# Kernel optimization log

Hardware: AMD Instinct MI355X
Metric: run time of the kernel (lower is better)

## Reference

```python
import jax, jax.numpy as jnp
import numpy as np

B, H, S, D = 8, 16, 1024, 64

def setup_inputs() -> dict:
    key = jax.random.key(0)
    k1, k2, k3, k4 = jax.random.split(key, 4)
    Q = jax.random.normal(k1, (B, H, S, D), dtype=jnp.float32)
    K = jax.random.normal(k2, (B, H, S, D), dtype=jnp.float32)
    V = jax.random.normal(k3, (B, H, S, D), dtype=jnp.float32)
    mask = jax.random.randint(k4, (B,), 0, 2).astype(jnp.bool_)
    return {"Q": Q, "K": K, "V": V, "mask": mask}

def reference(Q, K, V, mask):
    # scores: [B,H,S,S]
    scores = jnp.einsum('bhqd,bhkd->bhqk', Q, K)
    # per-batch-element mask broadcast over heads and both seq dims
    scores = jnp.where(mask[:, None, None, None], jnp.float32(-1e9), scores)
    # NOTE: original divides by sqrt(d) AFTER masking, so masked value is -1e9/sqrt(d)
    inv_sqrt_d = jnp.float32(1.0 / np.sqrt(Q.shape[-1]))
    attn = jax.nn.softmax(scores * inv_sqrt_d, axis=-1)
    return jnp.einsum('bhqk,bhkd->bhqd', attn, V)
```

## Files before the change

### kernel.cpp

```cpp
#include <hip/hip_runtime.h>
#include <hip/hip_bf16.h>

typedef __bf16 bf16;
typedef __bf16 bf16x4 __attribute__((ext_vector_type(4)));
typedef __bf16 bf16x8 __attribute__((ext_vector_type(8)));
typedef float  f32x16 __attribute__((ext_vector_type(16)));

#define S_  1024
#define D_  64
#define BQ  256
#define BK  64
#define KT  (S_/BK)
#define QT  (S_/BQ)
#define LD  72

#define ZERO16 {0.f,0.f,0.f,0.f,0.f,0.f,0.f,0.f,0.f,0.f,0.f,0.f,0.f,0.f,0.f,0.f}

__global__ __launch_bounds__(256, 2)
void fa_fwd(const float* __restrict__ Q, const float* __restrict__ K,
            const float* __restrict__ V, const int* __restrict__ mask,
            float* __restrict__ O)
{
    __shared__ bf16 ks[2][BK][LD];
    __shared__ bf16 vt[2][D_][LD];

    const int tid  = threadIdx.x;
    const int lane = tid & 63;
    const int w    = tid >> 6;
    const int l32  = lane & 31;
    const int hi   = lane >> 5;

    const int bid   = blockIdx.x;
    const int xcd   = bid & 7;
    const int rnd   = bid >> 3;
    const int qtile = rnd & 3;
    const int bh    = ((rnd >> 2) << 3) | xcd;
    const int b     = bh >> 4;
    const size_t base = (size_t)bh * (S_ * D_);
    const int qW = qtile * BQ + w * 64;

    const float qscale = (mask[b] != 0) ? 0.0f : 0.1803368801111204f;

    bf16x8 qf[2][4];
    #pragma unroll
    for (int nt = 0; nt < 2; ++nt) {
        const float* qp = Q + base + (size_t)(qW + nt * 32 + l32) * D_ + hi * 8;
        #pragma unroll
        for (int kc = 0; kc < 4; ++kc) {
            float4 a = *(const float4*)(qp + kc * 16);
            float4 c = *(const float4*)(qp + kc * 16 + 4);
            bf16x8 f;
            f[0] = (bf16)(a.x * qscale); f[1] = (bf16)(a.y * qscale);
            f[2] = (bf16)(a.z * qscale); f[3] = (bf16)(a.w * qscale);
            f[4] = (bf16)(c.x * qscale); f[5] = (bf16)(c.y * qscale);
            f[6] = (bf16)(c.z * qscale); f[7] = (bf16)(c.w * qscale);
            qf[nt][kc] = f;
        }
    }

    f32x16 o[2][2];
    #pragma unroll
    for (int dm = 0; dm < 2; ++dm)
        #pragma unroll
        for (int nt = 0; nt < 2; ++nt) o[dm][nt] = (f32x16)ZERO16;
    float lsum[2] = {0.f, 0.f};

    const int vkq = (tid >> 2) & 15;
    const int vkp = (vkq & 12) | ((vkq & 1) << 1) | ((vkq >> 1) & 1);
    const int vc4 = (tid & 3) + 4 * w;
    const float4* gk = (const float4*)(K + base);
    const float4* gv = (const float4*)(V + base);

    float4 kr[4], vr[4];
    #pragma unroll
    for (int it = 0; it < 4; ++it) kr[it] = gk[it * 256 + tid];
    #pragma unroll
    for (int r = 0; r < 4; ++r)    vr[r]  = gv[(vkq * 4 + r) * 16 + vc4];

    auto mkpf = [&](const f32x16& sv, bf16x8& fA, bf16x8& fB, float& ls) {
        bf16x8 a, c;
        #pragma unroll
        for (int i = 0; i < 8; ++i) {
            float e0 = __builtin_amdgcn_exp2f(sv[i]);
            float e1 = __builtin_amdgcn_exp2f(sv[8 + i]);
            ls += e0 + e1;
            a[i] = (bf16)e0;
            c[i] = (bf16)e1;
        }
        fA = a; fB = c;
    };

    for (int kt = 0; kt < KT; ++kt) {
        bf16 (*ksb)[LD] = ks[kt & 1];
        bf16 (*vtb)[LD] = vt[kt & 1];

        #pragma unroll
        for (int it = 0; it < 4; ++it) {
            int i = it * 256 + tid;
            int row = i >> 4, c4 = i & 15;
            bf16x4 hk = {(bf16)kr[it].x, (bf16)kr[it].y, (bf16)kr[it].z, (bf16)kr[it].w};
            *(bf16x4*)&ksb[row][c4 * 4] = hk;
        }
        {
            bf16x4 t0 = {(bf16)vr[0].x, (bf16)vr[1].x, (bf16)vr[2].x, (bf16)vr[3].x};
            bf16x4 t1 = {(bf16)vr[0].y, (bf16)vr[1].y, (bf16)vr[2].y, (bf16)vr[3].y};
            bf16x4 t2 = {(bf16)vr[0].z, (bf16)vr[1].z, (bf16)vr[2].z, (bf16)vr[3].z};
            bf16x4 t3 = {(bf16)vr[0].w, (bf16)vr[1].w, (bf16)vr[2].w, (bf16)vr[3].w};
            *(bf16x4*)&vtb[vc4 * 4 + 0][vkp * 4] = t0;
            *(bf16x4*)&vtb[vc4 * 4 + 1][vkp * 4] = t1;
            *(bf16x4*)&vtb[vc4 * 4 + 2][vkp * 4] = t2;
            *(bf16x4*)&vtb[vc4 * 4 + 3][vkp * 4] = t3;
        }
        {
            int ktn = (kt + 1 < KT) ? (kt + 1) : kt;
            #pragma unroll
            for (int it = 0; it < 4; ++it) kr[it] = gk[ktn * 1024 + it * 256 + tid];
            #pragma unroll
            for (int r = 0; r < 4; ++r)    vr[r]  = gv[ktn * 1024 + (vkq * 4 + r) * 16 + vc4];
        }
        __syncthreads();

        f32x16 s00 = ZERO16, s01 = ZERO16, s10 = ZERO16, s11 = ZERO16;
        #pragma unroll
        for (int kc = 0; kc < 4; ++kc) {
            bf16x8 k0 = *(const bf16x8*)&ksb[l32][kc * 16 + hi * 8];
            bf16x8 k1 = *(const bf16x8*)&ksb[32 + l32][kc * 16 + hi * 8];
            s00 = __builtin_amdgcn_mfma_f32_32x32x16_bf16(k0, qf[0][kc], s00, 0, 0, 0);
            s01 = __builtin_amdgcn_mfma_f32_32x32x16_bf16(k0, qf[1][kc], s01, 0, 0, 0);
            s10 = __builtin_amdgcn_mfma_f32_32x32x16_bf16(k1, qf[0][kc], s10, 0, 0, 0);
            s11 = __builtin_amdgcn_mfma_f32_32x32x16_bf16(k1, qf[1][kc], s11, 0, 0, 0);
        }

        bf16x8 pf[4][2];
        mkpf(s00, pf[0][0], pf[1][0], lsum[0]);
        mkpf(s01, pf[0][1], pf[1][1], lsum[1]);
        mkpf(s10, pf[2][0], pf[3][0], lsum[0]);
        mkpf(s11, pf[2][1], pf[3][1], lsum[1]);

        #pragma unroll
        for (int kc = 0; kc < 4; ++kc) {
            bf16x8 v0 = *(const bf16x8*)&vtb[l32][kc * 16 + hi * 8];
            bf16x8 v1 = *(const bf16x8*)&vtb[32 + l32][kc * 16 + hi * 8];
            o[0][0] = __builtin_amdgcn_mfma_f32_32x32x16_bf16(v0, pf[kc][0], o[0][0], 0, 0, 0);
            o[0][1] = __builtin_amdgcn_mfma_f32_32x32x16_bf16(v0, pf[kc][1], o[0][1], 0, 0, 0);
            o[1][0] = __builtin_amdgcn_mfma_f32_32x32x16_bf16(v1, pf[kc][0], o[1][0], 0, 0, 0);
            o[1][1] = __builtin_amdgcn_mfma_f32_32x32x16_bf16(v1, pf[kc][1], o[1][1], 0, 0, 0);
        }
    }

    #pragma unroll
    for (int nt = 0; nt < 2; ++nt) {
        float lv = lsum[nt] + __shfl_xor(lsum[nt], 32);
        float inv = 1.0f / lv;
        float* op = O + base + (size_t)(qW + nt * 32 + l32) * D_ + hi * 4;
        #pragma unroll
        for (int g = 0; g < 4; ++g) {
            float4 a = { o[0][nt][g * 4 + 0] * inv, o[0][nt][g * 4 + 1] * inv,
                         o[0][nt][g * 4 + 2] * inv, o[0][nt][g * 4 + 3] * inv };
            *(float4*)(op + g * 8) = a;
            float4 c = { o[1][nt][g * 4 + 0] * inv, o[1][nt][g * 4 + 1] * inv,
                         o[1][nt][g * 4 + 2] * inv, o[1][nt][g * 4 + 3] * inv };
            *(float4*)(op + 32 + g * 8) = c;
        }
    }
}

extern "C" void kernel_launch(void* const* d_in, const int* in_sizes, int n_in,
                              void* d_out, int out_size, void* d_ws, size_t ws_size,
                              hipStream_t stream)
{
    const float* Q    = (const float*)d_in[0];
    const float* K    = (const float*)d_in[1];
    const float* V    = (const float*)d_in[2];
    const int*   mask = (const int*)d_in[3];
    float*       O    = (float*)d_out;

    dim3 grid(8 * 16 * QT);
    fa_fwd<<<grid, 256, 0, stream>>>(Q, K, V, mask, O);
}
```

Before: 150.0 us.

## Split key sequence across two thread groups and merge partial outputs via LDS

Each block now runs 512 threads in two groups of 256. Each group processes half of the key/value tiles with its own double-buffered LDS staging, and the partial outputs and row sums are combined through shared memory at the end. The split is exact because the kernel uses no running max, so partial sums just add. The aim is to double the waves available per block for hiding latency without changing the grid size. The cost is extra LDS traffic and barriers for the merge, and possibly more register pressure under the 512-thread launch bound.

```diff
diff --git a/kernel.cpp b/kernel.cpp
--- a/kernel.cpp
+++ b/kernel.cpp
@@ -10,25 +10,29 @@
 #define D_  64
 #define BQ  256
 #define BK  64
-#define KT  (S_/BK)
+#define GKT 8
 #define QT  (S_/BQ)
 #define LD  72
 
 #define ZERO16 {0.f,0.f,0.f,0.f,0.f,0.f,0.f,0.f,0.f,0.f,0.f,0.f,0.f,0.f,0.f,0.f}
 
-__global__ __launch_bounds__(256, 2)
+__global__ __launch_bounds__(512, 4)
 void fa_fwd(const float* __restrict__ Q, const float* __restrict__ K,
             const float* __restrict__ V, const int* __restrict__ mask,
             float* __restrict__ O)
 {
-    __shared__ bf16 ks[2][BK][LD];
-    __shared__ bf16 vt[2][D_][LD];
+    __shared__ __align__(16) char smem[2][2][2 * BK * LD * sizeof(bf16)];
 
     const int tid  = threadIdx.x;
+    const int g    = tid >> 8;
+    const int tl   = tid & 255;
     const int lane = tid & 63;
-    const int w    = tid >> 6;
+    const int w    = (tid >> 6) & 3;
     const int l32  = lane & 31;
     const int hi   = lane >> 5;
+
+    bf16 (*ks)[BK][LD] = (bf16(*)[BK][LD])smem[g][0];
+    bf16 (*vt)[BK][LD] = (bf16(*)[BK][LD])smem[g][1];
 
     const int bid   = blockIdx.x;
     const int xcd   = bid & 7;
@@ -65,15 +69,15 @@
         for (int nt = 0; nt < 2; ++nt) o[dm][nt] = (f32x16)ZERO16;
     float lsum[2] = {0.f, 0.f};
 
-    const int vkq = (tid >> 2) & 15;
+    const int vkq = (tl >> 2) & 15;
     const int vkp = (vkq & 12) | ((vkq & 1) << 1) | ((vkq >> 1) & 1);
-    const int vc4 = (tid & 3) + 4 * w;
-    const float4* gk = (const float4*)(K + base);
-    const float4* gv = (const float4*)(V + base);
+    const int vc4 = (tl & 3) + 4 * w;
+    const float4* gk = (const float4*)(K + base) + (size_t)g * GKT * 1024;
+    const float4* gv = (const float4*)(V + base) + (size_t)g * GKT * 1024;
 
     float4 kr[4], vr[4];
     #pragma unroll
-    for (int it = 0; it < 4; ++it) kr[it] = gk[it * 256 + tid];
+    for (int it = 0; it < 4; ++it) kr[it] = gk[it * 256 + tl];
     #pragma unroll
     for (int r = 0; r < 4; ++r)    vr[r]  = gv[(vkq * 4 + r) * 16 + vc4];
 
@@ -90,13 +94,13 @@
         fA = a; fB = c;
     };
 
-    for (int kt = 0; kt < KT; ++kt) {
+    for (int kt = 0; kt < GKT; ++kt) {
         bf16 (*ksb)[LD] = ks[kt & 1];
         bf16 (*vtb)[LD] = vt[kt & 1];
 
         #pragma unroll
         for (int it = 0; it < 4; ++it) {
-            int i = it * 256 + tid;
+            int i = it * 256 + tl;
             int row = i >> 4, c4 = i & 15;
             bf16x4 hk = {(bf16)kr[it].x, (bf16)kr[it].y, (bf16)kr[it].z, (bf16)kr[it].w};
             *(bf16x4*)&ksb[row][c4 * 4] = hk;
@@ -112,9 +116,9 @@
             *(bf16x4*)&vtb[vc4 * 4 + 3][vkp * 4] = t3;
         }
         {
-            int ktn = (kt + 1 < KT) ? (kt + 1) : kt;
-            #pragma unroll
-            for (int it = 0; it < 4; ++it) kr[it] = gk[ktn * 1024 + it * 256 + tid];
+            int ktn = (kt + 1 < GKT) ? (kt + 1) : kt;
+            #pragma unroll
+            for (int it = 0; it < 4; ++it) kr[it] = gk[ktn * 1024 + it * 256 + tl];
             #pragma unroll
             for (int r = 0; r < 4; ++r)    vr[r]  = gv[ktn * 1024 + (vkq * 4 + r) * 16 + vc4];
         }
@@ -148,19 +152,55 @@
         }
     }
 
-    #pragma unroll
-    for (int nt = 0; nt < 2; ++nt) {
-        float lv = lsum[nt] + __shfl_xor(lsum[nt], 32);
-        float inv = 1.0f / lv;
-        float* op = O + base + (size_t)(qW + nt * 32 + l32) * D_ + hi * 4;
-        #pragma unroll
-        for (int g = 0; g < 4; ++g) {
-            float4 a = { o[0][nt][g * 4 + 0] * inv, o[0][nt][g * 4 + 1] * inv,
-                         o[0][nt][g * 4 + 2] * inv, o[0][nt][g * 4 + 3] * inv };
-            *(float4*)(op + g * 8) = a;
-            float4 c = { o[1][nt][g * 4 + 0] * inv, o[1][nt][g * 4 + 1] * inv,
-                         o[1][nt][g * 4 + 2] * inv, o[1][nt][g * 4 + 3] * inv };
-            *(float4*)(op + 32 + g * 8) = c;
+    float lv[2];
+    #pragma unroll
+    for (int nt = 0; nt < 2; ++nt)
+        lv[nt] = lsum[nt] + __shfl_xor(lsum[nt], 32);
+
+    __syncthreads();
+    float* oex = (float*)smem;
+    float* lex = oex + 16 * 256 * 4;
+
+    if (g == 1) {
+        #pragma unroll
+        for (int dm = 0; dm < 2; ++dm)
+            #pragma unroll
+            for (int nt = 0; nt < 2; ++nt)
+                #pragma unroll
+                for (int c = 0; c < 4; ++c) {
+                    int chunk = (dm * 2 + nt) * 4 + c;
+                    float4 v = { o[dm][nt][c * 4 + 0], o[dm][nt][c * 4 + 1],
+                                 o[dm][nt][c * 4 + 2], o[dm][nt][c * 4 + 3] };
+                    *(float4*)&oex[(chunk * 256 + tl) * 4] = v;
+                }
+        if (hi == 0) {
+            lex[w * 64 + l32]      = lv[0];
+            lex[w * 64 + 32 + l32] = lv[1];
+        }
+    }
+    __syncthreads();
+
+    if (g == 0) {
+        #pragma unroll
+        for (int nt = 0; nt < 2; ++nt) {
+            float lt  = lv[nt] + lex[w * 64 + nt * 32 + l32];
+            float inv = 1.0f / lt;
+            float* op = O + base + (size_t)(qW + nt * 32 + l32) * D_ + hi * 4;
+            #pragma unroll
+            for (int gg = 0; gg < 4; ++gg) {
+                float4 p0 = *(float4*)&oex[(((0 * 2 + nt) * 4 + gg) * 256 + tl) * 4];
+                float4 p1 = *(float4*)&oex[(((1 * 2 + nt) * 4 + gg) * 256 + tl) * 4];
+                float4 a = { (o[0][nt][gg * 4 + 0] + p0.x) * inv,
+                             (o[0][nt][gg * 4 + 1] + p0.y) * inv,
+                             (o[0][nt][gg * 4 + 2] + p0.z) * inv,
+                             (o[0][nt][gg * 4 + 3] + p0.w) * inv };
+                *(float4*)(op + gg * 8) = a;
+                float4 c = { (o[1][nt][gg * 4 + 0] + p1.x) * inv,
+                             (o[1][nt][gg * 4 + 1] + p1.y) * inv,
+                             (o[1][nt][gg * 4 + 2] + p1.z) * inv,
+                             (o[1][nt][gg * 4 + 3] + p1.w) * inv };
+                *(float4*)(op + 32 + gg * 8) = c;
+            }
         }
     }
 }
@@ -176,5 +216,5 @@
     float*       O    = (float*)d_out;
 
     dim3 grid(8 * 16 * QT);
-    fa_fwd<<<grid, 256, 0, stream>>>(Q, K, V, mask, O);
+    fa_fwd<<<grid, 512, 0, stream>>>(Q, K, V, mask, O);
 }
```

Result: slower. 573.6 us (+282.4%).
